# Optimization experiments

Measured on AMD Instinct MI355X. Metric: run time of the kernel, lower is better.

## Reference

```python
import jax, jax.numpy as jnp
import numpy as np

N = 8192
E = 262144
IN_SELF = 512
IN_AGG = 512
OUT = 256  # out_channels; hidden = 2*OUT = 512


def _glorot(key, shape, scale=0.05):
    return jax.random.normal(key, shape, dtype=jnp.float32) * scale


def setup_inputs() -> dict:
    key = jax.random.key(0)
    ks = jax.random.split(key, 16)
    x_self = jax.random.normal(ks[0], (N, IN_SELF), dtype=jnp.float32)
    x_neighbor = jax.random.normal(ks[1], (N, IN_AGG), dtype=jnp.float32)
    edge_index = jax.random.randint(ks[2], (2, E), 0, N, dtype=jnp.int64)
    H = 2 * OUT
    return {
        "x_self": x_self,
        "x_neighbor": x_neighbor,
        "edge_index": edge_index,
        # linear_in_self: IN_SELF -> 2*OUT
        "w_in_self": _glorot(ks[3], (IN_SELF, H)),
        "b_in_self": jnp.zeros((H,), jnp.float32),
        # linear_out_self: IN_SELF + 2*OUT -> OUT
        "w_out_self": _glorot(ks[4], (IN_SELF + H, OUT)),
        "b_out_self": jnp.zeros((OUT,), jnp.float32),
        # gcn1: IN_SELF -> 2*OUT
        "gw1": _glorot(ks[5], (IN_SELF, H)),
        "gb1": jnp.zeros((H,), jnp.float32),
        # gcn2: 2*OUT -> OUT
        "gw2": _glorot(ks[6], (H, OUT)),
        "gb2": jnp.zeros((OUT,), jnp.float32),
        # linear_out: IN_AGG + OUT -> OUT
        "w_out": _glorot(ks[7], (IN_AGG + OUT, OUT)),
        "b_out": jnp.zeros((OUT,), jnp.float32),
    }


def _gcn_norm(edge_index, n):
    # PyG GCNConv default: add self loops, symmetric deg^-1/2 normalization.
    loop = jnp.arange(n, dtype=edge_index.dtype)
    src = jnp.concatenate([edge_index[0], loop])
    dst = jnp.concatenate([edge_index[1], loop])
    deg = jax.ops.segment_sum(jnp.ones_like(dst, dtype=jnp.float32), dst, num_segments=n)
    dinv = jnp.where(deg > 0, jax.lax.rsqrt(deg), 0.0)
    norm = dinv[src] * dinv[dst]  # [E+N]
    return src, dst, norm


def _gcn(x, w, b, src, dst, norm, n):
    h = x @ w                                   # [N, out]
    msg = h[src] * norm[:, None]                # gather + scale
    agg = jax.ops.segment_sum(msg, dst, num_segments=n)
    return agg + b


def reference(x_self, x_neighbor, edge_index,
              w_in_self, b_in_self, w_out_self, b_out_self,
              gw1, gb1, gw2, gb2, w_out, b_out):
    n = x_self.shape[0]
    src, dst, norm = _gcn_norm(edge_index, n)
    # linear branch
    l1 = jax.nn.relu(x_self @ w_in_self + b_in_self)
    l1 = jnp.concatenate([x_self, l1], axis=1) @ w_out_self + b_out_self
    # GCN branch
    g1 = _gcn(x_self, gw1, gb1, src, dst, norm, n)
    g2 = _gcn(g1, gw2, gb2, src, dst, norm, n)
    x2 = jnp.concatenate([x_neighbor, g2], axis=1) @ w_out + b_out
    # concat latent, dense inner-product decode
    z = jnp.concatenate([l1, x2], axis=1)       # [N, 2*OUT]
    return jax.nn.sigmoid(z @ z.T)              # [N, N]
```

## Files before the change

### kernel.cpp

```cpp
#include <hip/hip_runtime.h>
#include <cstdint>
#include <cstddef>

#define NNODE 8192
#define NEDGE 262144

typedef __attribute__((ext_vector_type(8))) short bf16x8;
typedef __attribute__((ext_vector_type(4))) float f32x4;

__device__ __forceinline__ unsigned short f2bf_rn(float x) {
    unsigned u = __float_as_uint(x);
    u = (u + 0x7FFFu + ((u >> 16) & 1u)) >> 16;
    return (unsigned short)u;
}
__device__ __forceinline__ float bf2f(unsigned short h) {
    return __uint_as_float(((unsigned)h) << 16);
}

__device__ __forceinline__ void gload16(const char* gp, char* lp) {
    __builtin_amdgcn_global_load_lds((const __attribute__((address_space(1))) void*)gp,
                                     (__attribute__((address_space(3))) void*)lp, 16, 0, 0);
}


__global__ void k_count(const int* __restrict__ dst, int* __restrict__ cnt, int n) {
    int i = blockIdx.x * blockDim.x + threadIdx.x;
    if (i < n) atomicAdd(&cnt[dst[i]], 1);
}

__global__ __launch_bounds__(256) void k_scan(const int* __restrict__ cnt,
                                              int* __restrict__ row_start,
                                              int* __restrict__ cursor,
                                              float* __restrict__ dinv) {
    __shared__ int part[256];
    const int tid = threadIdx.x;
    const int PER = NNODE / 256;
    const int base = tid * PER;
    int loc[PER];
    int sum = 0;
#pragma unroll
    for (int i = 0; i < PER; ++i) { loc[i] = cnt[base + i]; sum += loc[i]; }
    part[tid] = sum;
    __syncthreads();
    if (tid == 0) {
        int r = 0;
        for (int i = 0; i < 256; ++i) { int t = part[i]; part[i] = r; r += t; }
    }
    __syncthreads();
    int run = part[tid];
#pragma unroll
    for (int i = 0; i < PER; ++i) {
        row_start[base + i] = run;
        cursor[base + i] = run;
        dinv[base + i] = rsqrtf((float)loc[i] + 1.0f);
        run += loc[i];
    }
    if (tid == 255) row_start[NNODE] = run;
}

__global__ void k_fill_csr2(const int* __restrict__ src, const int* __restrict__ dst,
                            int* __restrict__ cursor, const float* __restrict__ dinv,
                            int* __restrict__ slist, float* __restrict__ wlist, int n) {
    int e = blockIdx.x * blockDim.x + threadIdx.x;
    if (e < n) {
        int d = dst[e];
        int s = src[e];
        int pos = atomicAdd(&cursor[d], 1);
        slist[pos] = s;
        wlist[pos] = dinv[s] * dinv[d];
    }
}

__device__ __forceinline__ void split_wt_tile(const float* __restrict__ W, int K, int N,
                                              int k0, int n0,
                                              unsigned short* __restrict__ Oh,
                                              unsigned short* __restrict__ Ol,
                                              float (*t)[33]) {
    const int c = threadIdx.x & 31, r8 = threadIdx.x >> 5;
#pragma unroll
    for (int i = 0; i < 4; ++i) {
        int r = r8 + i * 8;
        t[r][c] = W[(size_t)(k0 + r) * N + n0 + c];
    }
    __syncthreads();
#pragma unroll
    for (int i = 0; i < 4; ++i) {
        int r = r8 + i * 8;
        float x = t[c][r];
        unsigned short h = f2bf_rn(x);
        Oh[(size_t)(n0 + r) * K + k0 + c] = h;
        Ol[(size_t)(n0 + r) * K + k0 + c] = f2bf_rn(x - bf2f(h));
    }
}

__global__ __launch_bounds__(256) void k_prep(
    const float* __restrict__ x_self, const float* __restrict__ x_neighbor,
    const float* __restrict__ w_in_self, const float* __restrict__ w_out_self,
    const float* __restrict__ w_out, const float* __restrict__ gw1,
    const float* __restrict__ gw2, const float* __restrict__ gb1,
    unsigned short* __restrict__ xsh, unsigned short* __restrict__ xsl,
    unsigned short* __restrict__ xnh, unsigned short* __restrict__ xnl,
    unsigned short* __restrict__ wAt_h, unsigned short* __restrict__ wAt_l,
    unsigned short* __restrict__ wost_h, unsigned short* __restrict__ wost_l,
    unsigned short* __restrict__ wot_h, unsigned short* __restrict__ wot_l,
    float* __restrict__ bc, int* __restrict__ cnt) {
    __shared__ float t[32][33];
    const int b = blockIdx.x;
    const int tid = threadIdx.x;
    if (b < 8192) {
        const float* src = (b < 4096) ? x_self : x_neighbor;
        unsigned short* oh = (b < 4096) ? xsh : xnh;
        unsigned short* ol = (b < 4096) ? xsl : xnl;
        const int i = (b & 4095) * 256 + tid;
        float4 v = ((const float4*)src)[i];
        float x[4] = {v.x, v.y, v.z, v.w};
        unsigned short h[4], l[4];
#pragma unroll
        for (int j = 0; j < 4; ++j) {
            h[j] = f2bf_rn(x[j]);
            l[j] = f2bf_rn(x[j] - bf2f(h[j]));
        }
        ((ushort4*)oh)[i] = make_ushort4(h[0], h[1], h[2], h[3]);
        ((ushort4*)ol)[i] = make_ushort4(l[0], l[1], l[2], l[3]);
    } else if (b < 8448) {
        const int b2 = b - 8192;
        split_wt_tile(w_in_self, 512, 512, (b2 & 15) * 32, (b2 >> 4) * 32, wAt_h, wAt_l, t);
    } else if (b < 8576) {
        const int b3 = b - 8448;
        const int k0 = (b3 & 15) * 32, n0 = (b3 >> 4) * 32;
        const int nloc = tid & 31, kg = tid >> 5;
        float a[4] = {0.f, 0.f, 0.f, 0.f};
        for (int c = 0; c < 512; ++c) {
            float g2v = gw2[(size_t)c * 256 + n0 + nloc];
#pragma unroll
            for (int i = 0; i < 4; ++i)
                a[i] += gw1[(size_t)(k0 + kg * 4 + i) * 512 + c] * g2v;
        }
#pragma unroll
        for (int i = 0; i < 4; ++i) {
            unsigned short hh = f2bf_rn(a[i]);
            wAt_h[(size_t)(512 + n0 + nloc) * 512 + k0 + kg * 4 + i] = hh;
            wAt_l[(size_t)(512 + n0 + nloc) * 512 + k0 + kg * 4 + i] = f2bf_rn(a[i] - bf2f(hh));
        }
    } else if (b < 8832) {
        const int b4 = b - 8576;
        split_wt_tile(w_out_self, 1024, 256, (b4 & 31) * 32, (b4 >> 5) * 32, wost_h, wost_l, t);
    } else if (b < 9024) {
        const int b5 = b - 8832;
        split_wt_tile(w_out, 768, 256, (b5 % 24) * 32, (b5 / 24) * 32, wot_h, wot_l, t);
    } else if (b == 9024) {
        float a = 0.0f;
        for (int c = 0; c < 512; ++c) a += gb1[c] * gw2[(size_t)c * 256 + tid];
        bc[tid] = a;
    } else {
        cnt[(b - 9025) * 256 + tid] = 0;
    }
}

__device__ __forceinline__ void stage_g(char* buf,
                                        const char* aH, const char* aL, size_t strA,
                                        const char* bH, const char* bL, size_t strB,
                                        int rloc, int w) {
#pragma unroll
    for (int i = 0; i < 2; ++i) {
        const size_t r = (size_t)(rloc + i * 64);
        char* lp = buf + i * 4096 + w * 1024;
        gload16(aH + r * strA, lp);
        gload16(aL + r * strA, lp + 8192);
    }
    gload16(bH + (size_t)rloc * strB, buf + 16384 + w * 1024);
    gload16(bL + (size_t)rloc * strB, buf + 20480 + w * 1024);
}

__device__ __forceinline__ void core_2x4(const char* cur, int w, int sread, int lane,
                                         f32x4 acc[2][4]) {
    bf16x8 ah[2], al[2], bh[4], bl[4];
#pragma unroll
    for (int m = 0; m < 2; ++m) {
        const int row = w * 32 + m * 16 + (lane & 15);
        ah[m] = *(const bf16x8*)(cur + row * 64 + sread);
        al[m] = *(const bf16x8*)(cur + 8192 + row * 64 + sread);
    }
#pragma unroll
    for (int n = 0; n < 4; ++n) {
        const int row = n * 16 + (lane & 15);
        bh[n] = *(const bf16x8*)(cur + 16384 + row * 64 + sread);
        bl[n] = *(const bf16x8*)(cur + 20480 + row * 64 + sread);
    }
#pragma unroll
    for (int m = 0; m < 2; ++m)
#pragma unroll
        for (int n = 0; n < 4; ++n) {
            acc[m][n] = __builtin_amdgcn_mfma_f32_16x16x32_bf16(ah[m], bh[n], acc[m][n], 0, 0, 0);
            acc[m][n] = __builtin_amdgcn_mfma_f32_16x16x32_bf16(ah[m], bl[n], acc[m][n], 0, 0, 0);
            acc[m][n] = __builtin_amdgcn_mfma_f32_16x16x32_bf16(al[m], bh[n], acc[m][n], 0, 0, 0);
        }
}

__global__ __launch_bounds__(256) void k_gemm128_A(
    const unsigned short* __restrict__ xsh, const unsigned short* __restrict__ xsl,
    const unsigned short* __restrict__ wAt_h, const unsigned short* __restrict__ wAt_l,
    const float* __restrict__ bias,
    unsigned short* __restrict__ l1h, unsigned short* __restrict__ l1l,
    float* __restrict__ hc) {
    __shared__ __align__(16) char smem[49152];
    const int tid = threadIdx.x, lane = tid & 63, w = tid >> 6;
    const int t0 = blockIdx.x;
    const int s = (t0 & 7) * 96 + (t0 >> 3);
    const int bm = (s / 12) * 128, bn = (s % 12) * 64;
    const int rloc = w * 16 + (lane >> 2);
    const int swz_src = ((lane & 3) ^ ((lane >> 3) & 3)) * 16;
    const int sread = ((lane >> 4) ^ ((lane >> 1) & 3)) * 16;
    const char* Ah = (const char*)xsh + (size_t)bm * 1024 + swz_src;
    const char* Al = (const char*)xsl + (size_t)bm * 1024 + swz_src;
    const char* Bh = (const char*)wAt_h + (size_t)bn * 1024 + swz_src;
    const char* Bl = (const char*)wAt_l + (size_t)bn * 1024 + swz_src;

    f32x4 acc[2][4] = {};
    stage_g(smem,         Ah,      Al,      1024, Bh,      Bl,      1024, rloc, w);
    stage_g(smem + 24576, Ah + 64, Al + 64, 1024, Bh + 64, Bl + 64, 1024, rloc, w);
    for (int ks = 0; ks < 16; ++ks) {
        if (ks < 15) asm volatile("s_waitcnt vmcnt(6)" ::: "memory");
        else         asm volatile("s_waitcnt vmcnt(0)" ::: "memory");
        __builtin_amdgcn_s_barrier();
        __builtin_amdgcn_sched_barrier(0);
        core_2x4(smem + (ks & 1) * 24576, w, sread, lane, acc);
        __builtin_amdgcn_sched_barrier(0);
        __builtin_amdgcn_s_barrier();
        if (ks < 14) {
            const int kb = (ks + 2) * 64;
            stage_g(smem + (ks & 1) * 24576, Ah + kb, Al + kb, 1024,
                    Bh + kb, Bl + kb, 1024, rloc, w);
        }
    }

    const int rj = (lane >> 4) * 4, cc = lane & 15;
#pragma unroll
    for (int m = 0; m < 2; ++m) {
#pragma unroll
        for (int n = 0; n < 4; ++n) {
            const int col = bn + n * 16 + cc;
#pragma unroll
            for (int j = 0; j < 4; ++j) {
                const int row = bm + w * 32 + m * 16 + rj + j;
                float x = acc[m][n][j];
                if (col < 512) {
                    x += bias[col];
                    x = fmaxf(x, 0.0f);
                    unsigned short h = f2bf_rn(x);
                    l1h[(size_t)row * 512 + col] = h;
                    l1l[(size_t)row * 512 + col] = f2bf_rn(x - bf2f(h));
                } else {
                    hc[(size_t)row * 256 + (col - 512)] = x;
                }
            }
        }
    }
}

__global__ __launch_bounds__(256) void k_gemm128_Z(
    const unsigned short* __restrict__ xsh, const unsigned short* __restrict__ xsl,
    const unsigned short* __restrict__ l1h, const unsigned short* __restrict__ l1l,
    const unsigned short* __restrict__ xnh, const unsigned short* __restrict__ xnl,
    const unsigned short* __restrict__ g2h, const unsigned short* __restrict__ g2l,
    const unsigned short* __restrict__ wost_h, const unsigned short* __restrict__ wost_l,
    const unsigned short* __restrict__ wot_h, const unsigned short* __restrict__ wot_l,
    const float* __restrict__ b_out_self, const float* __restrict__ b_out,
    unsigned short* __restrict__ zhi, unsigned short* __restrict__ zlo) {
    __shared__ __align__(16) char smem[49152];
    const int t0 = blockIdx.x;
    const int s = (t0 & 7) * 64 + (t0 >> 3);
    const int half = s >> 8;
    const int rem = s & 255;
    const int bn = (rem & 3) * 64;
    const int bm = (rem >> 2) * 128;
    const int tid = threadIdx.x, lane = tid & 63, w = tid >> 6;
    const int rloc = w * 16 + (lane >> 2);
    const int swz_src = ((lane & 3) ^ ((lane >> 3) & 3)) * 16;
    const int sread = ((lane >> 4) ^ ((lane >> 1) & 3)) * 16;

    const unsigned short *A1h, *A1l, *A2h, *A2l, *Wh, *Wl;
    const float* bias;
    int Ktot;
    size_t strA2, strB;
    if (half == 0) {
        A1h = xsh; A1l = xsl; A2h = l1h; A2l = l1l; strA2 = 1024;
        Wh = wost_h; Wl = wost_l; strB = 2048; Ktot = 1024; bias = b_out_self;
    } else {
        A1h = xnh; A1l = xnl; A2h = g2h; A2l = g2l; strA2 = 512;
        Wh = wot_h; Wl = wot_l; strB = 1536; Ktot = 768; bias = b_out;
    }
    const int nsteps = Ktot / 32;
    const char* Bh = (const char*)Wh + (size_t)bn * strB + swz_src;
    const char* Bl = (const char*)Wl + (size_t)bn * strB + swz_src;

    auto asrc = [&](int k0, const char*& sh, const char*& sl, size_t& st) {
        if (k0 < 512) {
            sh = (const char*)A1h + (size_t)bm * 1024 + (size_t)k0 * 2 + swz_src;
            sl = (const char*)A1l + (size_t)bm * 1024 + (size_t)k0 * 2 + swz_src;
            st = 1024;
        } else {
            sh = (const char*)A2h + (size_t)bm * strA2 + (size_t)(k0 - 512) * 2 + swz_src;
            sl = (const char*)A2l + (size_t)bm * strA2 + (size_t)(k0 - 512) * 2 + swz_src;
            st = strA2;
        }
    };

    f32x4 acc[2][4] = {};
    {
        const char *sh, *sl; size_t st;
        asrc(0, sh, sl, st);
        stage_g(smem, sh, sl, st, Bh, Bl, strB, rloc, w);
        asrc(32, sh, sl, st);
        stage_g(smem + 24576, sh, sl, st, Bh + 64, Bl + 64, strB, rloc, w);
    }
    for (int ks = 0; ks < nsteps; ++ks) {
        if (ks < nsteps - 1) asm volatile("s_waitcnt vmcnt(6)" ::: "memory");
        else                 asm volatile("s_waitcnt vmcnt(0)" ::: "memory");
        __builtin_amdgcn_s_barrier();
        __builtin_amdgcn_sched_barrier(0);
        core_2x4(smem + (ks & 1) * 24576, w, sread, lane, acc);
        __builtin_amdgcn_sched_barrier(0);
        __builtin_amdgcn_s_barrier();
        if (ks + 2 < nsteps) {
            const char *sh, *sl; size_t st;
            asrc((ks + 2) * 32, sh, sl, st);
            stage_g(smem + (ks & 1) * 24576, sh, sl, st,
                    Bh + (size_t)(ks + 2) * 64, Bl + (size_t)(ks + 2) * 64, strB, rloc, w);
        }
    }

    const int rj = (lane >> 4) * 4, cc = lane & 15;
    const int zoff = half * 256;
#pragma unroll
    for (int m = 0; m < 2; ++m) {
#pragma unroll
        for (int n = 0; n < 4; ++n) {
            const int col = bn + n * 16 + cc;
            const float bv = bias[col];
#pragma unroll
            for (int j = 0; j < 4; ++j) {
                const int row = bm + w * 32 + m * 16 + rj + j;
                float x = acc[m][n][j] + bv;
                unsigned short h = f2bf_rn(x);
                zhi[(size_t)row * 512 + zoff + col] = h;
                zlo[(size_t)row * 512 + zoff + col] = f2bf_rn(x - bf2f(h));
            }
        }
    }
}

template <int MODE>
__global__ __launch_bounds__(256) void k_agg2(
    const int* __restrict__ row_start, const int* __restrict__ slist,
    const float* __restrict__ wlist, const float* __restrict__ dinv,
    const float* __restrict__ h,
    const float* __restrict__ bc, const float* __restrict__ b2,
    float* __restrict__ outf,
    unsigned short* __restrict__ oh, unsigned short* __restrict__ ol) {
    const int n = blockIdx.x;
    const int c = threadIdx.x;
    const float di = dinv[n];
    float acc = di * di * h[(size_t)n * 256 + c];
    float sv = di * di;
    const int e0 = row_start[n], e1 = row_start[n + 1];
    int j = e0;
    for (; j + 8 <= e1; j += 8) {
        int ss[8];
        float ww[8], vv[8];
#pragma unroll
        for (int u = 0; u < 8; ++u) { ss[u] = slist[j + u]; ww[u] = wlist[j + u]; }
#pragma unroll
        for (int u = 0; u < 8; ++u) vv[u] = h[(size_t)ss[u] * 256 + c];
#pragma unroll
        for (int u = 0; u < 8; ++u) {
            acc += ww[u] * vv[u];
            if (MODE) sv += ww[u];
        }
    }
    for (; j < e1; ++j) {
        const float wv = wlist[j];
        acc += wv * h[(size_t)slist[j] * 256 + c];
        if (MODE) sv += wv;
    }
    if (MODE == 0) {
        outf[(size_t)n * 256 + c] = acc;
    } else {
        float x = acc + sv * bc[c] + b2[c];
        unsigned short hb = f2bf_rn(x);
        oh[(size_t)n * 256 + c] = hb;
        ol[(size_t)n * 256 + c] = f2bf_rn(x - bf2f(hb));
    }
}

__device__ __forceinline__ void zzt_stage(char* buf, const char* s0, const char* s1,
                                          const char* s2, const char* s3,
                                          int rloc, int swz_src, int w, int kbyte) {
    const char* srcs[4] = {s0, s1, s2, s3};
#pragma unroll
    for (int tile = 0; tile < 4; ++tile) {
#pragma unroll
        for (int i = 0; i < 2; ++i) {
            const char* gp = srcs[tile] + (size_t)(rloc + i * 64) * 1024 + kbyte + swz_src;
            char* lp = buf + tile * 8192 + i * 4096 + w * 1024;
            gload16(gp, lp);
        }
    }
}

__global__ __launch_bounds__(256) void k_zzt_mfma(const unsigned short* __restrict__ zhi,
                                                  const unsigned short* __restrict__ zlo,
                                                  float* __restrict__ out) {
    __shared__ __align__(16) char smem[65536];
    const int tid = threadIdx.x;
    const int lane = tid & 63;
    const int w = tid >> 6;
    const int wr = w >> 1, wc = w & 1;

    const int t0 = blockIdx.x;
    const int t = (t0 & 7) * 260 + (t0 >> 3);
    int bi = (int)((sqrtf(8.0f * (float)t + 1.0f) - 1.0f) * 0.5f);
    while ((bi + 1) * (bi + 2) / 2 <= t) ++bi;
    while (bi * (bi + 1) / 2 > t) --bi;
    const int bj = t - bi * (bi + 1) / 2;

    const char* s0 = (const char*)zhi + (size_t)(bi * 128) * 1024;
    const char* s1 = (const char*)zlo + (size_t)(bi * 128) * 1024;
    const char* s2 = (const char*)zhi + (size_t)(bj * 128) * 1024;
    const char* s3 = (const char*)zlo + (size_t)(bj * 128) * 1024;

    const int rloc = w * 16 + (lane >> 2);
    const int swz_src = ((lane & 3) ^ ((lane >> 3) & 3)) * 16;
    const int sread = ((lane >> 4) ^ ((lane >> 1) & 3)) * 16;

    f32x4 acc[4][4] = {};

    zzt_stage(smem,         s0, s1, s2, s3, rloc, swz_src, w, 0);
    zzt_stage(smem + 32768, s0, s1, s2, s3, rloc, swz_src, w, 64);

    for (int ks = 0; ks < 16; ++ks) {
        if (ks < 15) asm volatile("s_waitcnt vmcnt(8)" ::: "memory");
        else         asm volatile("s_waitcnt vmcnt(0)" ::: "memory");
        __builtin_amdgcn_s_barrier();
        __builtin_amdgcn_sched_barrier(0);
        const char* cur = smem + (ks & 1) * 32768;

        bf16x8 ah[4], al[4], bh[4], bl[4];
        const char* pa = cur + (wr * 64 + (lane & 15)) * 64 + sread;
        const char* pb = cur + 16384 + (wc * 64 + (lane & 15)) * 64 + sread;
#pragma unroll
        for (int m = 0; m < 4; ++m) {
            ah[m] = *(const bf16x8*)(pa + m * 1024);
            al[m] = *(const bf16x8*)(pa + 8192 + m * 1024);
        }
#pragma unroll
        for (int n = 0; n < 4; ++n) {
            bh[n] = *(const bf16x8*)(pb + n * 1024);
            bl[n] = *(const bf16x8*)(pb + 8192 + n * 1024);
        }
        __builtin_amdgcn_s_setprio(1);
#pragma unroll
        for (int m = 0; m < 4; ++m)
#pragma unroll
            for (int n = 0; n < 4; ++n) {
                acc[m][n] = __builtin_amdgcn_mfma_f32_16x16x32_bf16(ah[m], bh[n], acc[m][n], 0, 0, 0);
                acc[m][n] = __builtin_amdgcn_mfma_f32_16x16x32_bf16(ah[m], bl[n], acc[m][n], 0, 0, 0);
                acc[m][n] = __builtin_amdgcn_mfma_f32_16x16x32_bf16(al[m], bh[n], acc[m][n], 0, 0, 0);
            }
        __builtin_amdgcn_s_setprio(0);
        __builtin_amdgcn_sched_barrier(0);
        __builtin_amdgcn_s_barrier();
        if (ks < 14)
            zzt_stage(smem + (ks & 1) * 32768, s0, s1, s2, s3, rloc, swz_src, w,
                      (ks + 2) * 64);
    }

    const int rj = (lane >> 4) * 4;
    const int cc = lane & 15;
#pragma unroll
    for (int m = 0; m < 4; ++m) {
#pragma unroll
        for (int n = 0; n < 4; ++n) {
            float s[4];
#pragma unroll
            for (int j = 0; j < 4; ++j)
                s[j] = 1.0f / (1.0f + __expf(-acc[m][n][j]));
            const int gr0 = bi * 128 + wr * 64 + m * 16 + rj;
            const int gc  = bj * 128 + wc * 64 + n * 16 + cc;
#pragma unroll
            for (int j = 0; j < 4; ++j)
                __builtin_nontemporal_store(s[j], out + (size_t)(gr0 + j) * NNODE + gc);
            if (bi != bj) {
                const int mr = bj * 128 + wc * 64 + n * 16 + cc;
                const int mc = bi * 128 + wr * 64 + m * 16 + rj;
                f32x4 v = {s[0], s[1], s[2], s[3]};
                __builtin_nontemporal_store(v, (f32x4*)(out + (size_t)mr * NNODE + mc));
            }
        }
    }
}

extern "C" void kernel_launch(void* const* d_in, const int* in_sizes, int n_in,
                              void* d_out, int out_size, void* d_ws, size_t ws_size,
                              hipStream_t stream) {
    const float* x_self     = (const float*)d_in[0];
    const float* x_neighbor = (const float*)d_in[1];
    const int*   ei         = (const int*)d_in[2];
    const float* w_in_self  = (const float*)d_in[3];
    const float* b_in_self  = (const float*)d_in[4];
    const float* w_out_self = (const float*)d_in[5];
    const float* b_out_self = (const float*)d_in[6];
    const float* gw1        = (const float*)d_in[7];
    const float* gb1        = (const float*)d_in[8];
    const float* gw2        = (const float*)d_in[9];
    const float* gb2        = (const float*)d_in[10];
    const float* w_out      = (const float*)d_in[11];
    const float* b_out      = (const float*)d_in[12];
    float* out = (float*)d_out;

    char* ws = (char*)d_ws;
    const size_t MB = 1024 * 1024;
    const size_t KB = 1024;
    int*   cnt       = (int*)(ws + 0);
    int*   row_start = (int*)(ws + 32 * KB);
    int*   cursor    = (int*)(ws + 96 * KB);
    float* dinv      = (float*)(ws + 128 * KB);
    float* bc        = (float*)(ws + 192 * KB);
    int*   slist     = (int*)(ws + 2 * MB);
    float* wlist     = (float*)(ws + 3 * MB);
    unsigned short* xsh = (unsigned short*)(ws + 4 * MB);
    unsigned short* xsl = (unsigned short*)(ws + 12 * MB);
    unsigned short* xnh = (unsigned short*)(ws + 20 * MB);
    unsigned short* xnl = (unsigned short*)(ws + 28 * MB);
    unsigned short* l1h = (unsigned short*)(ws + 36 * MB);
    unsigned short* l1l = (unsigned short*)(ws + 44 * MB);
    float*          hc  = (float*)(ws + 52 * MB);
    float*          t1  = (float*)(ws + 60 * MB);
    unsigned short* g2h = (unsigned short*)(ws + 68 * MB);
    unsigned short* g2l = (unsigned short*)(ws + 72 * MB);
    unsigned short* zhi = (unsigned short*)(ws + 76 * MB);
    unsigned short* zlo = (unsigned short*)(ws + 84 * MB);
    unsigned short* wAt_h = (unsigned short*)(ws + 92 * MB);
    unsigned short* wAt_l = (unsigned short*)(ws + 93 * MB);
    unsigned short* wost_h = (unsigned short*)(ws + 94 * MB);
    unsigned short* wost_l = (unsigned short*)(ws + 95 * MB);
    unsigned short* wot_h  = (unsigned short*)(ws + 96 * MB);
    unsigned short* wot_l  = (unsigned short*)(ws + 97 * MB);

    const int* srcA = ei;
    const int* dstA = ei + NEDGE;

    k_prep<<<9057, 256, 0, stream>>>(x_self, x_neighbor, w_in_self, w_out_self, w_out,
                                     gw1, gw2, gb1, xsh, xsl, xnh, xnl,
                                     wAt_h, wAt_l, wost_h, wost_l, wot_h, wot_l, bc, cnt);

    k_count<<<NEDGE / 256, 256, 0, stream>>>(dstA, cnt, NEDGE);
    k_scan<<<1, 256, 0, stream>>>(cnt, row_start, cursor, dinv);
    k_fill_csr2<<<NEDGE / 256, 256, 0, stream>>>(srcA, dstA, cursor, dinv, slist, wlist, NEDGE);

    k_gemm128_A<<<768, 256, 0, stream>>>(
        xsh, xsl, wAt_h, wAt_l, b_in_self, l1h, l1l, hc);

    k_agg2<0><<<NNODE, 256, 0, stream>>>(row_start, slist, wlist, dinv, hc,
                                         nullptr, nullptr, t1, nullptr, nullptr);
    k_agg2<1><<<NNODE, 256, 0, stream>>>(row_start, slist, wlist, dinv, t1,
                                         bc, gb2, nullptr, g2h, g2l);

    k_gemm128_Z<<<512, 256, 0, stream>>>(
        xsh, xsl, l1h, l1l, xnh, xnl, g2h, g2l,
        wost_h, wost_l, wot_h, wot_l, b_out_self, b_out, zhi, zlo);

    k_zzt_mfma<<<2080, 256, 0, stream>>>(zhi, zlo, out);
}
```

Measured before the change: 371.5 us.

## Use 128x256 rectangular tiles for the symmetric Z·Zᵀ decode kernel

Replaces the triangular 128x128 tile scheduling of the sigmoid(Z·Zᵀ) kernel with 128x256 rectangular tiles that cover the lower triangle, writing both each tile and its mirror. Each wave now computes 8x4 MFMA fragments, so every staged A/B slice is reused across more output. This cuts LDS and global staging traffic per output and halves the number of blocks. In exchange it uses 96KB of shared memory with one block per CU. Near the diagonal some output blocks are computed and written twice.

```diff
diff --git a/kernel.cpp b/kernel.cpp
--- a/kernel.cpp
+++ b/kernel.cpp
@@ -393,109 +393,104 @@
     }
 }
 
-__device__ __forceinline__ void zzt_stage(char* buf, const char* s0, const char* s1,
-                                          const char* s2, const char* s3,
-                                          int rloc, int swz_src, int w, int kbyte) {
-    const char* srcs[4] = {s0, s1, s2, s3};
-#pragma unroll
-    for (int tile = 0; tile < 4; ++tile) {
-#pragma unroll
-        for (int i = 0; i < 2; ++i) {
-            const char* gp = srcs[tile] + (size_t)(rloc + i * 64) * 1024 + kbyte + swz_src;
-            char* lp = buf + tile * 8192 + i * 4096 + w * 1024;
-            gload16(gp, lp);
-        }
-    }
-}
-
-__global__ __launch_bounds__(256) void k_zzt_mfma(const unsigned short* __restrict__ zhi,
-                                                  const unsigned short* __restrict__ zlo,
-                                                  float* __restrict__ out) {
-    __shared__ __align__(16) char smem[65536];
+__global__ __launch_bounds__(256, 1) void k_zzt_rect(const unsigned short* __restrict__ zhi,
+                                                     const unsigned short* __restrict__ zlo,
+                                                     float* __restrict__ out) {
+    __shared__ __align__(16) char smem[98304];
     const int tid = threadIdx.x;
     const int lane = tid & 63;
     const int w = tid >> 6;
-    const int wr = w >> 1, wc = w & 1;
 
     const int t0 = blockIdx.x;
-    const int t = (t0 & 7) * 260 + (t0 >> 3);
-    int bi = (int)((sqrtf(8.0f * (float)t + 1.0f) - 1.0f) * 0.5f);
-    while ((bi + 1) * (bi + 2) / 2 <= t) ++bi;
-    while (bi * (bi + 1) / 2 > t) --bi;
-    const int bj = t - bi * (bi + 1) / 2;
-
-    const char* s0 = (const char*)zhi + (size_t)(bi * 128) * 1024;
-    const char* s1 = (const char*)zlo + (size_t)(bi * 128) * 1024;
-    const char* s2 = (const char*)zhi + (size_t)(bj * 128) * 1024;
-    const char* s3 = (const char*)zlo + (size_t)(bj * 128) * 1024;
-
-    const int rloc = w * 16 + (lane >> 2);
+    int p = (t0 & 7) * 132 + (t0 >> 3);
+    int J = 0;
+    while (p >= 64 - 2 * J) { p -= 64 - 2 * J; ++J; }
+    const int I = 2 * J + p;
+
+    const char* pp0 = (const char*)zhi + (size_t)(I * 128) * 1024;
+    const char* pp1 = (const char*)zlo + (size_t)(I * 128) * 1024;
+    const char* pp2 = (const char*)zhi + (size_t)(J * 256) * 1024;
+    const char* pp3 = (const char*)zlo + (size_t)(J * 256) * 1024;
+
     const int swz_src = ((lane & 3) ^ ((lane >> 3) & 3)) * 16;
     const int sread = ((lane >> 4) ^ ((lane >> 1) & 3)) * 16;
 
-    f32x4 acc[4][4] = {};
-
-    zzt_stage(smem,         s0, s1, s2, s3, rloc, swz_src, w, 0);
-    zzt_stage(smem + 32768, s0, s1, s2, s3, rloc, swz_src, w, 64);
+    auto STAGE = [&](int buf, int kt) {
+        const int kb = kt * 64;
+        char* base = smem + buf * 49152;
+        const char* pp[4] = {pp0, pp1, pp2, pp3};
+#pragma unroll
+        for (int jj = 0; jj < 12; ++jj) {
+            const int c = w * 12 + jj;
+            int q, ci;
+            char* dst;
+            if (c < 16) {
+                q = c >> 3; ci = c & 7;
+                dst = base + q * 8192 + ci * 1024;
+            } else {
+                const int c2 = c - 16;
+                q = 2 + (c2 >> 4); ci = c2 & 15;
+                dst = base + 16384 + (c2 >> 4) * 16384 + ci * 1024;
+            }
+            gload16(pp[q] + (size_t)(ci * 16 + (lane >> 2)) * 1024 + kb + swz_src, dst);
+        }
+    };
+
+    f32x4 acc[8][4] = {};
+
+    STAGE(0, 0);
+    STAGE(1, 1);
 
     for (int ks = 0; ks < 16; ++ks) {
-        if (ks < 15) asm volatile("s_waitcnt vmcnt(8)" ::: "memory");
+        if (ks < 15) asm volatile("s_waitcnt vmcnt(12)" ::: "memory");
         else         asm volatile("s_waitcnt vmcnt(0)" ::: "memory");
         __builtin_amdgcn_s_barrier();
         __builtin_amdgcn_sched_barrier(0);
-        const char* cur = smem + (ks & 1) * 32768;
-
-        bf16x8 ah[4], al[4], bh[4], bl[4];
-        const char* pa = cur + (wr * 64 + (lane & 15)) * 64 + sread;
-        const char* pb = cur + 16384 + (wc * 64 + (lane & 15)) * 64 + sread;
-#pragma unroll
-        for (int m = 0; m < 4; ++m) {
-            ah[m] = *(const bf16x8*)(pa + m * 1024);
-            al[m] = *(const bf16x8*)(pa + 8192 + m * 1024);
-        }
+        const char* cur = smem + (ks & 1) * 49152;
+
+        bf16x8 bh[4], bl[4];
 #pragma unroll
         for (int n = 0; n < 4; ++n) {
-            bh[n] = *(const bf16x8*)(pb + n * 1024);
-            bl[n] = *(const bf16x8*)(pb + 8192 + n * 1024);
-        }
-        __builtin_amdgcn_s_setprio(1);
-#pragma unroll
-        for (int m = 0; m < 4; ++m)
+            const int cr = w * 64 + n * 16 + (lane & 15);
+            bh[n] = *(const bf16x8*)(cur + 16384 + cr * 64 + sread);
+            bl[n] = *(const bf16x8*)(cur + 32768 + cr * 64 + sread);
+        }
+#pragma unroll
+        for (int m = 0; m < 8; ++m) {
+            const int row = m * 16 + (lane & 15);
+            bf16x8 ah = *(const bf16x8*)(cur + row * 64 + sread);
+            bf16x8 al = *(const bf16x8*)(cur + 8192 + row * 64 + sread);
+            __builtin_amdgcn_s_setprio(1);
 #pragma unroll
             for (int n = 0; n < 4; ++n) {
-                acc[m][n] = __builtin_amdgcn_mfma_f32_16x16x32_bf16(ah[m], bh[n], acc[m][n], 0, 0, 0);
-                acc[m][n] = __builtin_amdgcn_mfma_f32_16x16x32_bf16(ah[m], bl[n], acc[m][n], 0, 0, 0);
-                acc[m][n] = __builtin_amdgcn_mfma_f32_16x16x32_bf16(al[m], bh[n], acc[m][n], 0, 0, 0);
+                acc[m][n] = __builtin_amdgcn_mfma_f32_16x16x32_bf16(ah, bh[n], acc[m][n], 0, 0, 0);
+                acc[m][n] = __builtin_amdgcn_mfma_f32_16x16x32_bf16(ah, bl[n], acc[m][n], 0, 0, 0);
+                acc[m][n] = __builtin_amdgcn_mfma_f32_16x16x32_bf16(al, bh[n], acc[m][n], 0, 0, 0);
             }
-        __builtin_amdgcn_s_setprio(0);
+            __builtin_amdgcn_s_setprio(0);
+        }
         __builtin_amdgcn_sched_barrier(0);
         __builtin_amdgcn_s_barrier();
-        if (ks < 14)
-            zzt_stage(smem + (ks & 1) * 32768, s0, s1, s2, s3, rloc, swz_src, w,
-                      (ks + 2) * 64);
+        if (ks < 14) STAGE(ks & 1, ks + 2);
     }
 
     const int rj = (lane >> 4) * 4;
     const int cc = lane & 15;
 #pragma unroll
-    for (int m = 0; m < 4; ++m) {
+    for (int m = 0; m < 8; ++m) {
 #pragma unroll
         for (int n = 0; n < 4; ++n) {
             float s[4];
 #pragma unroll
             for (int j = 0; j < 4; ++j)
                 s[j] = 1.0f / (1.0f + __expf(-acc[m][n][j]));
-            const int gr0 = bi * 128 + wr * 64 + m * 16 + rj;
-            const int gc  = bj * 128 + wc * 64 + n * 16 + cc;
+            const int gr0 = I * 128 + m * 16 + rj;
+            const int gc  = J * 256 + w * 64 + n * 16 + cc;
 #pragma unroll
             for (int j = 0; j < 4; ++j)
                 __builtin_nontemporal_store(s[j], out + (size_t)(gr0 + j) * NNODE + gc);
-            if (bi != bj) {
-                const int mr = bj * 128 + wc * 64 + n * 16 + cc;
-                const int mc = bi * 128 + wr * 64 + m * 16 + rj;
-                f32x4 v = {s[0], s[1], s[2], s[3]};
-                __builtin_nontemporal_store(v, (f32x4*)(out + (size_t)mr * NNODE + mc));
-            }
+            f32x4 v = {s[0], s[1], s[2], s[3]};
+            __builtin_nontemporal_store(v, (f32x4*)(out + (size_t)gc * NNODE + gr0));
         }
     }
 }
@@ -570,5 +565,5 @@
         xsh, xsl, l1h, l1l, xnh, xnl, g2h, g2l,
         wost_h, wost_l, wot_h, wot_l, b_out_self, b_out, zhi, zlo);
 
-    k_zzt_mfma<<<2080, 256, 0, stream>>>(zhi, zlo, out);
-}
+    k_zzt_rect<<<1056, 256, 0, stream>>>(zhi, zlo, out);
+}
```

Result: slower. 410.9 us (+10.6%).

## Store GCN intermediates in bf16 and aggregate four nodes per block

Applied to the files above, without the earlier changes.

The projected GCN features (hc) and the first aggregation output (t1) are now stored as single bf16 instead of fp32, which halves the bytes read by the gather-heavy aggregation kernels. The aggregation kernel assigns one wavefront per node with ushort4 loads of four channels per lane, so one block covers four nodes instead of one. The Z GEMM tile order is also interleaved so both halves run concurrently. The cost is reduced precision in the GCN branch, since the low-part correction used elsewhere is dropped for these tensors.

```diff
diff --git a/kernel.cpp b/kernel.cpp
--- a/kernel.cpp
+++ b/kernel.cpp
@@ -202,7 +202,7 @@
     const unsigned short* __restrict__ wAt_h, const unsigned short* __restrict__ wAt_l,
     const float* __restrict__ bias,
     unsigned short* __restrict__ l1h, unsigned short* __restrict__ l1l,
-    float* __restrict__ hc) {
+    unsigned short* __restrict__ hcb) {
     __shared__ __align__(16) char smem[49152];
     const int tid = threadIdx.x, lane = tid & 63, w = tid >> 6;
     const int t0 = blockIdx.x;
@@ -251,7 +251,7 @@
                     l1h[(size_t)row * 512 + col] = h;
                     l1l[(size_t)row * 512 + col] = f2bf_rn(x - bf2f(h));
                 } else {
-                    hc[(size_t)row * 256 + (col - 512)] = x;
+                    hcb[(size_t)row * 256 + (col - 512)] = f2bf_rn(x);
                 }
             }
         }
@@ -270,8 +270,8 @@
     __shared__ __align__(16) char smem[49152];
     const int t0 = blockIdx.x;
     const int s = (t0 & 7) * 64 + (t0 >> 3);
-    const int half = s >> 8;
-    const int rem = s & 255;
+    const int half = s & 1;
+    const int rem = s >> 1;
     const int bn = (rem & 3) * 64;
     const int bm = (rem >> 2) * 128;
     const int tid = threadIdx.x, lane = tid & 63, w = tid >> 6;
@@ -351,45 +351,73 @@
 }
 
 template <int MODE>
-__global__ __launch_bounds__(256) void k_agg2(
+__global__ __launch_bounds__(256) void k_agg4(
     const int* __restrict__ row_start, const int* __restrict__ slist,
     const float* __restrict__ wlist, const float* __restrict__ dinv,
-    const float* __restrict__ h,
+    const unsigned short* __restrict__ h,
     const float* __restrict__ bc, const float* __restrict__ b2,
-    float* __restrict__ outf,
+    unsigned short* __restrict__ t1,
     unsigned short* __restrict__ oh, unsigned short* __restrict__ ol) {
-    const int n = blockIdx.x;
-    const int c = threadIdx.x;
+    const int n = blockIdx.x * 4 + (threadIdx.x >> 6);
+    const int lane = threadIdx.x & 63;
+    const int c0 = lane * 4;
     const float di = dinv[n];
-    float acc = di * di * h[(size_t)n * 256 + c];
+
+    ushort4 selfv = ((const ushort4*)(h + (size_t)n * 256))[lane];
+    float acc[4];
+    acc[0] = di * di * bf2f(selfv.x);
+    acc[1] = di * di * bf2f(selfv.y);
+    acc[2] = di * di * bf2f(selfv.z);
+    acc[3] = di * di * bf2f(selfv.w);
     float sv = di * di;
+
     const int e0 = row_start[n], e1 = row_start[n + 1];
     int j = e0;
-    for (; j + 8 <= e1; j += 8) {
-        int ss[8];
-        float ww[8], vv[8];
-#pragma unroll
-        for (int u = 0; u < 8; ++u) { ss[u] = slist[j + u]; ww[u] = wlist[j + u]; }
-#pragma unroll
-        for (int u = 0; u < 8; ++u) vv[u] = h[(size_t)ss[u] * 256 + c];
-#pragma unroll
-        for (int u = 0; u < 8; ++u) {
-            acc += ww[u] * vv[u];
+    for (; j + 4 <= e1; j += 4) {
+        int ss[4];
+        float ww[4];
+        ushort4 rv[4];
+#pragma unroll
+        for (int u = 0; u < 4; ++u) { ss[u] = slist[j + u]; ww[u] = wlist[j + u]; }
+#pragma unroll
+        for (int u = 0; u < 4; ++u)
+            rv[u] = ((const ushort4*)(h + (size_t)ss[u] * 256))[lane];
+#pragma unroll
+        for (int u = 0; u < 4; ++u) {
+            acc[0] += ww[u] * bf2f(rv[u].x);
+            acc[1] += ww[u] * bf2f(rv[u].y);
+            acc[2] += ww[u] * bf2f(rv[u].z);
+            acc[3] += ww[u] * bf2f(rv[u].w);
             if (MODE) sv += ww[u];
         }
     }
     for (; j < e1; ++j) {
         const float wv = wlist[j];
-        acc += wv * h[(size_t)slist[j] * 256 + c];
+        ushort4 rv = ((const ushort4*)(h + (size_t)slist[j] * 256))[lane];
+        acc[0] += wv * bf2f(rv.x);
+        acc[1] += wv * bf2f(rv.y);
+        acc[2] += wv * bf2f(rv.z);
+        acc[3] += wv * bf2f(rv.w);
         if (MODE) sv += wv;
     }
+
     if (MODE == 0) {
-        outf[(size_t)n * 256 + c] = acc;
+        ushort4 o;
+        o.x = f2bf_rn(acc[0]); o.y = f2bf_rn(acc[1]);
+        o.z = f2bf_rn(acc[2]); o.w = f2bf_rn(acc[3]);
+        ((ushort4*)(t1 + (size_t)n * 256))[lane] = o;
     } else {
-        float x = acc + sv * bc[c] + b2[c];
-        unsigned short hb = f2bf_rn(x);
-        oh[(size_t)n * 256 + c] = hb;
-        ol[(size_t)n * 256 + c] = f2bf_rn(x - bf2f(hb));
+        ushort4 vh, vl;
+        float x0 = acc[0] + sv * bc[c0 + 0] + b2[c0 + 0];
+        float x1 = acc[1] + sv * bc[c0 + 1] + b2[c0 + 1];
+        float x2 = acc[2] + sv * bc[c0 + 2] + b2[c0 + 2];
+        float x3 = acc[3] + sv * bc[c0 + 3] + b2[c0 + 3];
+        vh.x = f2bf_rn(x0); vl.x = f2bf_rn(x0 - bf2f(vh.x));
+        vh.y = f2bf_rn(x1); vl.y = f2bf_rn(x1 - bf2f(vh.y));
+        vh.z = f2bf_rn(x2); vl.z = f2bf_rn(x2 - bf2f(vh.z));
+        vh.w = f2bf_rn(x3); vl.w = f2bf_rn(x3 - bf2f(vh.w));
+        ((ushort4*)(oh + (size_t)n * 256))[lane] = vh;
+        ((ushort4*)(ol + (size_t)n * 256))[lane] = vl;
     }
 }
 
@@ -534,8 +562,8 @@
     unsigned short* xnl = (unsigned short*)(ws + 28 * MB);
     unsigned short* l1h = (unsigned short*)(ws + 36 * MB);
     unsigned short* l1l = (unsigned short*)(ws + 44 * MB);
-    float*          hc  = (float*)(ws + 52 * MB);
-    float*          t1  = (float*)(ws + 60 * MB);
+    unsigned short* hcb = (unsigned short*)(ws + 52 * MB);
+    unsigned short* t1b = (unsigned short*)(ws + 60 * MB);
     unsigned short* g2h = (unsigned short*)(ws + 68 * MB);
     unsigned short* g2l = (unsigned short*)(ws + 72 * MB);
     unsigned short* zhi = (unsigned short*)(ws + 76 * MB);
@@ -559,12 +587,12 @@
     k_fill_csr2<<<NEDGE / 256, 256, 0, stream>>>(srcA, dstA, cursor, dinv, slist, wlist, NEDGE);
 
     k_gemm128_A<<<768, 256, 0, stream>>>(
-        xsh, xsl, wAt_h, wAt_l, b_in_self, l1h, l1l, hc);
-
-    k_agg2<0><<<NNODE, 256, 0, stream>>>(row_start, slist, wlist, dinv, hc,
-                                         nullptr, nullptr, t1, nullptr, nullptr);
-    k_agg2<1><<<NNODE, 256, 0, stream>>>(row_start, slist, wlist, dinv, t1,
-                                         bc, gb2, nullptr, g2h, g2l);
+        xsh, xsl, wAt_h, wAt_l, b_in_self, l1h, l1l, hcb);
+
+    k_agg4<0><<<NNODE / 4, 256, 0, stream>>>(row_start, slist, wlist, dinv, hcb,
+                                             nullptr, nullptr, t1b, nullptr, nullptr);
+    k_agg4<1><<<NNODE / 4, 256, 0, stream>>>(row_start, slist, wlist, dinv, t1b,
+                                             bc, gb2, nullptr, g2h, g2l);
 
     k_gemm128_Z<<<512, 256, 0, stream>>>(
         xsh, xsl, l1h, l1l, xnh, xnl, g2h, g2l,
```

Measured after the change: 354.2 us. 1.05x faster.
